# Kernel tuning notes

Measured on AMD Instinct MI355X. Metric: run time of the kernel, lower is better.

Reference implementation:

```python
import jax, jax.numpy as jnp
import numpy as np

B, D, NT, H, K = 4096, 112, 200, 512, 10
HID = 512
IN = 3 * D + NT + 1   # GRU input size = 537
M0 = H + 3 * D + NT   # MLP first-layer input = 1048


def setup_inputs() -> dict:
    key = jax.random.key(0)
    ks = jax.random.split(key, 9)
    def w(k, shape, fan):
        return jax.random.normal(k, shape, jnp.float32) / np.sqrt(fan).astype(np.float32)
    return {
        "z": jax.random.normal(ks[0], (B, D), jnp.float32),
        "c": jax.random.normal(ks[1], (B, D + NT), jnp.float32),
        "b": jax.random.uniform(ks[2], (B, D), jnp.float32),
        "m": jax.random.uniform(ks[3], (B, D), jnp.float32),
        "Wih": w(ks[4], (IN, 3 * H), IN),
        "Whh": w(ks[5], (H, 3 * H), H),
        "bih": jnp.zeros((3 * H,), jnp.float32),
        "bhh": jnp.zeros((3 * H,), jnp.float32),
        "W0": w(ks[6], (M0, HID), M0),
        "b0": jnp.zeros((HID,), jnp.float32),
        "W1": w(ks[7], (HID, HID), HID),
        "b1": jnp.zeros((HID,), jnp.float32),
        "W2": w(ks[8], (HID, 3 * K), HID),
        "b2": jnp.zeros((3 * K,), jnp.float32),
    }


def reference(z, c, b, m, Wih, Whh, bih, bhh, W0, b0, W1, b1, W2, b2):
    """AutoReg.logp: autoregressive GRU + MLP mixture-density head, gaussian base."""
    Bn = z.shape[0]
    const = jnp.concatenate([c, b, m], axis=1)          # [B, 3D+NT] fixed per step
    gi_const = const @ Wih[1:] + bih                    # input-proj of constant part
    w_z = Wih[0]                                        # [3H] weight for scalar z_t
    mlp_const = const @ W0[H:] + b0                     # const part of first MLP layer
    W0h = W0[:H]
    # teacher-forced previous-z sequence: z_0 = -1, then z[:, t-1]
    z_prev = jnp.concatenate([-jnp.ones((Bn, 1), z.dtype), z[:, :-1]], axis=1).T  # [D, B]

    def step(h, zt):  # h: [B,H], zt: [B]
        gi = zt[:, None] * w_z + gi_const               # [B, 3H]
        gh = h @ Whh + bhh
        ir, iz, inn = jnp.split(gi, 3, axis=1)
        hr, hz, hn = jnp.split(gh, 3, axis=1)
        r = jax.nn.sigmoid(ir + hr)
        u = jax.nn.sigmoid(iz + hz)
        n = jnp.tanh(inn + r * hn)
        h2 = (1.0 - u) * n + u * h                      # torch GRU update
        a = jnp.tanh(h2 @ W0h + mlp_const)              # Linear + Tanh on [h||c||b||m]
        a = jnp.tanh(a @ W1 + b1)
        p = a @ W2 + b2                                 # [B, 3K] mixture params
        return h2, p

    h0 = jnp.zeros((Bn, H), z.dtype)
    _, ps = jax.lax.scan(step, h0, z_prev)              # ps: [D, B, 3K]
    params = jnp.transpose(ps, (1, 0, 2))               # [B, D, 3K]

    logits, means, lsig = jnp.split(params, 3, axis=-1)
    sig = jnp.exp(lsig)
    t = z[..., None]
    log_norm = -lsig - 0.5 * np.float32(np.log(2.0 * np.pi))
    log_kern = -0.5 * jnp.square((t - means) / sig)
    ll = jax.nn.logsumexp(log_kern + log_norm + logits, axis=-1) \
         - jax.nn.logsumexp(logits, axis=-1)            # [B, D]

    query = m * (1.0 - b)
    mask = -jnp.sort(-query, axis=1)                    # descending sort values
    return jnp.sum(ll * mask, axis=1)                   # [B]
```

## Files before the change

kernel.cpp:

```cpp
#include <hip/hip_runtime.h>
#include <hip/hip_bf16.h>
#include <float.h>
#include <math.h>

#define BN   4096
#define DD   112
#define HH   512
#define G3   1536
#define CW   536
#define HIDD 512

typedef __attribute__((ext_vector_type(8))) short short8;
typedef __attribute__((ext_vector_type(4))) float float4v;

__device__ __forceinline__ unsigned short f2bf(float x) {
    __hip_bfloat16 h = __float2bfloat16(x);
    return *(unsigned short*)&h;
}

__global__ void build_const(const float* __restrict__ c, const float* __restrict__ b,
                            const float* __restrict__ m, float* __restrict__ out) {
    int idx = blockIdx.x * blockDim.x + threadIdx.x;
    if (idx >= BN * CW) return;
    int row = idx / CW, col = idx - row * CW;
    float v;
    if (col < 312)      v = c[row * 312 + col];
    else if (col < 424) v = b[row * 112 + (col - 312)];
    else                v = m[row * 112 + (col - 424)];
    out[idx] = v;
}

__global__ __launch_bounds__(256) void gemm_bias(const float* __restrict__ A,
        const float* __restrict__ W, const float* __restrict__ bias,
        float* __restrict__ C, int N) {
    __shared__ float As[8][64];
    __shared__ float Ws[8][64];
    const int tid = threadIdx.x;
    const int tx = tid & 15, ty = tid >> 4;
    const int rowBase = blockIdx.x * 64, colBase = blockIdx.y * 64;
    float acc[4][4] = {};
    for (int kb = 0; kb < CW; kb += 8) {
        int l = tid * 2;
        {
            int i = l >> 3, j = l & 7;
            As[j][i] = A[(rowBase + i) * CW + kb + j];
            int i2 = (l + 1) >> 3, j2 = (l + 1) & 7;
            As[j2][i2] = A[(rowBase + i2) * CW + kb + j2];
        }
        {
            int j = l >> 6, n = l & 63;
            Ws[j][n] = W[(kb + j) * N + colBase + n];
            int j2 = (l + 1) >> 6, n2 = (l + 1) & 63;
            Ws[j2][n2] = W[(kb + j2) * N + colBase + n2];
        }
        __syncthreads();
#pragma unroll
        for (int k = 0; k < 8; ++k) {
            float av[4], wv[4];
#pragma unroll
            for (int i = 0; i < 4; ++i) av[i] = As[k][ty * 4 + i];
#pragma unroll
            for (int j = 0; j < 4; ++j) wv[j] = Ws[k][tx * 4 + j];
#pragma unroll
            for (int i = 0; i < 4; ++i)
#pragma unroll
                for (int j = 0; j < 4; ++j) acc[i][j] += av[i] * wv[j];
        }
        __syncthreads();
    }
#pragma unroll
    for (int i = 0; i < 4; ++i) {
        int r = rowBase + ty * 4 + i;
#pragma unroll
        for (int j = 0; j < 4; ++j) {
            int cc = colBase + tx * 4 + j;
            C[r * N + cc] = acc[i][j] + bias[cc];
        }
    }
}

__global__ __launch_bounds__(256) void gemm_gicP(const float* __restrict__ A,
        const float* __restrict__ W, const float* __restrict__ bih,
        const float* __restrict__ bhh, float* __restrict__ gicP) {
    const int N = G3;
    __shared__ float As[8][64];
    __shared__ float Ws[8][64];
    const int tid = threadIdx.x;
    const int tx = tid & 15, ty = tid >> 4;
    const int rowBase = blockIdx.x * 64, colBase = blockIdx.y * 64;
    float acc[4][4] = {};
    for (int kb = 0; kb < CW; kb += 8) {
        int l = tid * 2;
        {
            int i = l >> 3, j = l & 7;
            As[j][i] = A[(rowBase + i) * CW + kb + j];
            int i2 = (l + 1) >> 3, j2 = (l + 1) & 7;
            As[j2][i2] = A[(rowBase + i2) * CW + kb + j2];
        }
        {
            int j = l >> 6, n = l & 63;
            Ws[j][n] = W[(kb + j) * N + colBase + n];
            int j2 = (l + 1) >> 6, n2 = (l + 1) & 63;
            Ws[j2][n2] = W[(kb + j2) * N + colBase + n2];
        }
        __syncthreads();
#pragma unroll
        for (int k = 0; k < 8; ++k) {
            float av[4], wv[4];
#pragma unroll
            for (int i = 0; i < 4; ++i) av[i] = As[k][ty * 4 + i];
#pragma unroll
            for (int j = 0; j < 4; ++j) wv[j] = Ws[k][tx * 4 + j];
#pragma unroll
            for (int i = 0; i < 4; ++i)
#pragma unroll
                for (int j = 0; j < 4; ++j) acc[i][j] += av[i] * wv[j];
        }
        __syncthreads();
    }
#pragma unroll
    for (int i = 0; i < 4; ++i) {
        int r = rowBase + ty * 4 + i;
        int ablock = r >> 5, mrem = r & 31, mt = mrem >> 4, mm = mrem & 15;
        int quad = mm >> 2, rg = mm & 3;
#pragma unroll
        for (int j = 0; j < 4; ++j) {
            int cc = colBase + tx * 4 + j;
            int g = cc >> 9, nrem = cc & 511, tile = nrem >> 4, l16 = nrem & 15;
            int wv = tile & 15, ii = tile >> 4;
            size_t off = ((((size_t)(ablock * 16 + wv) * 2 + ii) * 2 + mt) * 3 + g) * 256
                         + (quad * 16 + l16) * 4 + rg;
            gicP[off] = acc[i][j] + bih[cc] + ((g < 2) ? bhh[cc] : 0.0f);
        }
    }
}

__global__ void sort_mask(const float* __restrict__ b, const float* __restrict__ m,
                          float* __restrict__ maskbuf) {
    __shared__ float s[128];
    const int row = blockIdx.x, t = threadIdx.x;
    float v = -FLT_MAX;
    if (t < DD) v = m[row * DD + t] * (1.0f - b[row * DD + t]);
    s[t] = v;
    __syncthreads();
    for (int k = 2; k <= 128; k <<= 1) {
        for (int j = k >> 1; j > 0; j >>= 1) {
            int ixj = t ^ j;
            if (ixj > t) {
                bool up = ((t & k) == 0);
                float a = s[t], bb = s[ixj];
                if ((a > bb) == up) { s[t] = bb; s[ixj] = a; }
            }
            __syncthreads();
        }
    }
    if (t < DD) maskbuf[row * DD + t] = s[127 - t];
}

__global__ void pack_w(const float* __restrict__ src, unsigned short* __restrict__ dst,
                       int kchunks, int ldn, int ncols) {
    int bid = blockIdx.x;
    int nt = bid / kchunks, kc = bid - nt * kchunks;
    int lane = threadIdx.x;
    int quad = lane >> 4, l16 = lane & 15;
    int n = nt * 16 + l16;
    unsigned short v[8];
#pragma unroll
    for (int j = 0; j < 8; ++j) {
        int k = kc * 32 + quad * 8 + j;
        float f = (n < ncols) ? src[(size_t)k * ldn + n] : 0.0f;
        v[j] = f2bf(f);
    }
    unsigned short* p = dst + ((size_t)bid * 64 + lane) * 8;
#pragma unroll
    for (int j = 0; j < 8; ++j) p[j] = v[j];
}

__global__ __launch_bounds__(1024, 4) void gru_rec(
    const float* __restrict__ z, const float* __restrict__ Wih,
    const float* __restrict__ bhh, const float* __restrict__ gicP,
    const unsigned short* __restrict__ WhhP, unsigned short* __restrict__ h2g)
{
    __shared__ unsigned short h_bf[32 * 520];
    __shared__ float zbuf[113 * 32];

    const int tid = threadIdx.x;
    const int wave = tid >> 6, lane = tid & 63;
    const int quad = lane >> 4, l16 = lane & 15;
    const int rowBase = blockIdx.x * 32;

    for (int idx = tid; idx < 32 * 520; idx += 1024) h_bf[idx] = 0;
    for (int idx = tid; idx < 113 * 32; idx += 1024) {
        int tt = idx >> 5, r = idx & 31;
        zbuf[idx] = (tt == 0) ? -1.0f : z[(size_t)(rowBase + r) * DD + tt - 1];
    }

    int hcol[2];
    float wz0[2], wz1[2], wz2[2], bh2r[2];
#pragma unroll
    for (int i = 0; i < 2; ++i) {
        int hc = (wave + 16 * i) * 16 + l16;
        hcol[i] = hc;
        wz0[i] = Wih[hc]; wz1[i] = Wih[512 + hc]; wz2[i] = Wih[1024 + hc];
        bh2r[i] = bhh[1024 + hc];
    }
    float h_own[2][2][4];
#pragma unroll
    for (int i = 0; i < 2; ++i)
#pragma unroll
        for (int mt = 0; mt < 2; ++mt)
#pragma unroll
            for (int rg = 0; rg < 4; ++rg) h_own[i][mt][rg] = 0.0f;

    const float* gicW = gicP + (size_t)(blockIdx.x * 16 + wave) * 12 * 256;
    const short8* WhhF = (const short8*)WhhP;
    __syncthreads();

    for (int t = 0; t < DD; ++t) {
        float4v acc[3][2][2];
#pragma unroll
        for (int i = 0; i < 2; ++i)
#pragma unroll
            for (int mt = 0; mt < 2; ++mt) {
                acc[0][i][mt] = *(const float4v*)(gicW + ((i * 2 + mt) * 3 + 0) * 256 + lane * 4);
                acc[1][i][mt] = *(const float4v*)(gicW + ((i * 2 + mt) * 3 + 1) * 256 + lane * 4);
                acc[2][i][mt] = (float4v){0.f, 0.f, 0.f, 0.f};
            }
#pragma unroll 4
        for (int kc = 0; kc < 16; ++kc) {
            short8 af[2];
#pragma unroll
            for (int mt = 0; mt < 2; ++mt)
                af[mt] = *(const short8*)&h_bf[(mt * 16 + l16) * 520 + kc * 32 + quad * 8];
#pragma unroll
            for (int i = 0; i < 2; ++i) {
                int tile = wave + 16 * i;
#pragma unroll
                for (int g = 0; g < 3; ++g) {
                    short8 bf = WhhF[((tile + 32 * g) * 16 + kc) * 64 + lane];
#pragma unroll
                    for (int mt = 0; mt < 2; ++mt)
                        acc[g][i][mt] = __builtin_amdgcn_mfma_f32_16x16x32_bf16(af[mt], bf, acc[g][i][mt], 0, 0, 0);
                }
            }
        }
        __syncthreads();
#pragma unroll
        for (int i = 0; i < 2; ++i)
#pragma unroll
            for (int mt = 0; mt < 2; ++mt) {
                float4v gn = *(const float4v*)(gicW + ((i * 2 + mt) * 3 + 2) * 256 + lane * 4);
#pragma unroll
                for (int rg = 0; rg < 4; ++rg) {
                    int m = mt * 16 + quad * 4 + rg;
                    float zt = zbuf[t * 32 + m];
                    float r = 1.0f / (1.0f + __expf(-(acc[0][i][mt][rg] + zt * wz0[i])));
                    float u = 1.0f / (1.0f + __expf(-(acc[1][i][mt][rg] + zt * wz1[i])));
                    float xn = gn[rg] + zt * wz2[i] + r * (acc[2][i][mt][rg] + bh2r[i]);
                    float n = 1.0f - 2.0f / (__expf(2.0f * xn) + 1.0f);
                    float h2 = (1.0f - u) * n + u * h_own[i][mt][rg];
                    h_own[i][mt][rg] = h2;
                    h_bf[m * 520 + hcol[i]] = f2bf(h2);
                }
            }
        __syncthreads();
        {
            int flat = tid * 16;
            int r = flat >> 9, col = flat & 511;
            const uint4* src = (const uint4*)&h_bf[r * 520 + col];
            uint4 v0 = src[0], v1 = src[1];
            uint4* dst = (uint4*)&h2g[((size_t)(rowBase + r) * DD + t) * 512 + col];
            dst[0] = v0; dst[1] = v1;
        }
    }
}

__global__ __launch_bounds__(1024, 4) void head_mdn(
    const float* __restrict__ z, const float* __restrict__ b1,
    const float* __restrict__ b2, const float* __restrict__ mlp_const,
    const float* __restrict__ maskbuf, const unsigned short* __restrict__ h2g,
    const unsigned short* __restrict__ W0hP, const unsigned short* __restrict__ W1P,
    const unsigned short* __restrict__ W2P, float* __restrict__ out)
{
    __shared__ unsigned short h_bf[32 * 520];
    __shared__ unsigned short a_bf[32 * 520];
    __shared__ float pp[16 * 512];

    const int tid = threadIdx.x;
    const int wave = tid >> 6, lane = tid & 63;
    const int quad = lane >> 4, l16 = lane & 15;
    const int pr = tid >> 5, pc = tid & 31;
    const int bi = blockIdx.x / 7, ti = blockIdx.x - bi * 7;
    const int b0 = bi * 2, t0 = ti * 16;

    {
        int flat = tid * 16;
        int r = flat >> 9, col = flat & 511;
        int bb = b0 + (r >> 4), tt = t0 + (r & 15);
        const uint4* src = (const uint4*)&h2g[((size_t)bb * DD + tt) * 512 + col];
        uint4 v0 = src[0], v1 = src[1];
        uint4* dst = (uint4*)&h_bf[r * 520 + col];
        dst[0] = v0; dst[1] = v1;
    }
    int hcol[2];
    float b1c[2], mlc[2][2];
#pragma unroll
    for (int i = 0; i < 2; ++i) {
        int hc = (wave + 16 * i) * 16 + l16;
        hcol[i] = hc;
        b1c[i] = b1[hc];
#pragma unroll
        for (int mt = 0; mt < 2; ++mt) mlc[i][mt] = mlp_const[(size_t)(b0 + mt) * HIDD + hc];
    }
    const float b2v = (pc < 30) ? b2[pc] : 0.0f;
    const int mdn_mt = pr >> 4, mdn_m = pr & 15;
    const int ppofs = (mdn_mt * 8) * 512 + (pc >> 4) * 256
                      + ((mdn_m >> 2) * 16 + (pc & 15)) * 4 + (mdn_m & 3);

    const short8* W0hF = (const short8*)W0hP;
    const short8* W1F  = (const short8*)W1P;
    const short8* W2F  = (const short8*)W2P;
    __syncthreads();

    float4v acc1[2][2];
#pragma unroll
    for (int i = 0; i < 2; ++i)
#pragma unroll
        for (int mt = 0; mt < 2; ++mt)
            acc1[i][mt] = (float4v){mlc[i][mt], mlc[i][mt], mlc[i][mt], mlc[i][mt]};
#pragma unroll 4
    for (int kc = 0; kc < 16; ++kc) {
        short8 af0 = *(const short8*)&h_bf[l16 * 520 + kc * 32 + quad * 8];
        short8 af1 = *(const short8*)&h_bf[(16 + l16) * 520 + kc * 32 + quad * 8];
#pragma unroll
        for (int i = 0; i < 2; ++i) {
            short8 bf = W0hF[((wave + 16 * i) * 16 + kc) * 64 + lane];
            acc1[i][0] = __builtin_amdgcn_mfma_f32_16x16x32_bf16(af0, bf, acc1[i][0], 0, 0, 0);
            acc1[i][1] = __builtin_amdgcn_mfma_f32_16x16x32_bf16(af1, bf, acc1[i][1], 0, 0, 0);
        }
    }
#pragma unroll
    for (int i = 0; i < 2; ++i)
#pragma unroll
        for (int mt = 0; mt < 2; ++mt)
#pragma unroll
            for (int rg = 0; rg < 4; ++rg) {
                int m = mt * 16 + quad * 4 + rg;
                float x = acc1[i][mt][rg];
                a_bf[m * 520 + hcol[i]] = f2bf(1.0f - 2.0f / (__expf(2.0f * x) + 1.0f));
            }
    __syncthreads();
    float4v acc2[2][2];
#pragma unroll
    for (int i = 0; i < 2; ++i)
#pragma unroll
        for (int mt = 0; mt < 2; ++mt)
            acc2[i][mt] = (float4v){b1c[i], b1c[i], b1c[i], b1c[i]};
#pragma unroll 4
    for (int kc = 0; kc < 16; ++kc) {
        short8 af0 = *(const short8*)&a_bf[l16 * 520 + kc * 32 + quad * 8];
        short8 af1 = *(const short8*)&a_bf[(16 + l16) * 520 + kc * 32 + quad * 8];
#pragma unroll
        for (int i = 0; i < 2; ++i) {
            short8 bf = W1F[((wave + 16 * i) * 16 + kc) * 64 + lane];
            acc2[i][0] = __builtin_amdgcn_mfma_f32_16x16x32_bf16(af0, bf, acc2[i][0], 0, 0, 0);
            acc2[i][1] = __builtin_amdgcn_mfma_f32_16x16x32_bf16(af1, bf, acc2[i][1], 0, 0, 0);
        }
    }
    __syncthreads();
#pragma unroll
    for (int i = 0; i < 2; ++i)
#pragma unroll
        for (int mt = 0; mt < 2; ++mt)
#pragma unroll
            for (int rg = 0; rg < 4; ++rg) {
                int m = mt * 16 + quad * 4 + rg;
                float x = acc2[i][mt][rg];
                a_bf[m * 520 + hcol[i]] = f2bf(1.0f - 2.0f / (__expf(2.0f * x) + 1.0f));
            }
    __syncthreads();
    {
        const int mtw = wave >> 3;
        float4v ap0 = (float4v){0.f, 0.f, 0.f, 0.f}, ap1 = (float4v){0.f, 0.f, 0.f, 0.f};
#pragma unroll
        for (int kk = 0; kk < 2; ++kk) {
            int kc = (wave & 7) * 2 + kk;
            short8 af = *(const short8*)&a_bf[(mtw * 16 + l16) * 520 + kc * 32 + quad * 8];
            ap0 = __builtin_amdgcn_mfma_f32_16x16x32_bf16(af, W2F[(0 * 16 + kc) * 64 + lane], ap0, 0, 0, 0);
            ap1 = __builtin_amdgcn_mfma_f32_16x16x32_bf16(af, W2F[(1 * 16 + kc) * 64 + lane], ap1, 0, 0, 0);
        }
#pragma unroll
        for (int rg = 0; rg < 4; ++rg) {
            pp[wave * 512 + 0 * 256 + lane * 4 + rg] = ap0[rg];
            pp[wave * 512 + 1 * 256 + lane * 4 + rg] = ap1[rg];
        }
    }
    __syncthreads();
    float llm;
    {
        float pv = b2v;
#pragma unroll
        for (int w = 0; w < 8; ++w) pv += pp[ppofs + w * 512];
        const int half = lane & 32;
        float meanv = __shfl(pv, half + ((pc + 10) & 31), 64);
        float lsigv = __shfl(pv, half + ((pc + 20) & 31), 64);
        float e1, e2;
        if (pc < 10) {
            float ztar = z[(size_t)(b0 + mdn_mt) * DD + t0 + mdn_m];
            float invs = __expf(-lsigv);
            float dd = (ztar - meanv) * invs;
            e1 = -0.5f * dd * dd - lsigv - 0.91893853320467274f + pv;
            e2 = pv;
        } else { e1 = -FLT_MAX; e2 = -FLT_MAX; }
        float m1 = e1, m2 = e2;
#pragma unroll
        for (int off = 16; off > 0; off >>= 1) {
            m1 = fmaxf(m1, __shfl_xor(m1, off, 64));
            m2 = fmaxf(m2, __shfl_xor(m2, off, 64));
        }
        float s1 = (pc < 10) ? __expf(e1 - m1) : 0.0f;
        float s2 = (pc < 10) ? __expf(e2 - m2) : 0.0f;
#pragma unroll
        for (int off = 16; off > 0; off >>= 1) {
            s1 += __shfl_xor(s1, off, 64);
            s2 += __shfl_xor(s2, off, 64);
        }
        float ll = (m1 + __logf(s1)) - (m2 + __logf(s2));
        llm = ll * maskbuf[(size_t)(b0 + mdn_mt) * DD + t0 + mdn_m];
    }
    __syncthreads();
    if (pc == 0) pp[pr] = llm;
    __syncthreads();
    if (tid < 2) {
        float s = 0.0f;
#pragma unroll
        for (int j = 0; j < 16; ++j) s += pp[tid * 16 + j];
        atomicAdd(&out[b0 + tid], s);
    }
}

__global__ __launch_bounds__(1024, 4) void gru_mfma_r5(
    const float* __restrict__ z, const float* __restrict__ Wih,
    const float* __restrict__ bhh, const float* __restrict__ b1,
    const float* __restrict__ b2,
    const float* __restrict__ gi_const, const float* __restrict__ mlp_const,
    const float* __restrict__ maskbuf,
    const unsigned short* __restrict__ WhhP, const unsigned short* __restrict__ W0hP,
    const unsigned short* __restrict__ W1P, const unsigned short* __restrict__ W2P,
    float* __restrict__ out)
{
    __shared__ unsigned short h_bf[16 * 520];
    __shared__ unsigned short a_bf[16 * 520];
    __shared__ float pp[16 * 512];
    __shared__ float zbuf[113 * 16];
    __shared__ float mbuf[16 * 112];

    const int tid = threadIdx.x;
    const int wave = tid >> 6, lane = tid & 63;
    const int quad = lane >> 4, l16 = lane & 15;
    const int pr = tid >> 5, pc = tid & 31;
    const int rowBase = blockIdx.x * 16;

    for (int idx = tid; idx < 16 * 520; idx += 1024) h_bf[idx] = 0;
    for (int idx = tid; idx < 113 * 16; idx += 1024) {
        int tt = idx >> 4, r = idx & 15;
        zbuf[idx] = (tt == 0) ? -1.0f : z[(rowBase + r) * DD + tt - 1];
    }
    for (int idx = tid; idx < 16 * 112; idx += 1024) {
        int r = idx / DD, tt = idx - r * DD;
        mbuf[idx] = maskbuf[(rowBase + r) * DD + tt];
    }
    int hcol[2];
    float wz0[2], wz1[2], wz2[2], bh2r[2], b1c[2];
    float gic0[2][4], gic1[2][4], gic2[2][4], mlc[2][4];
    float h_own[2][4];
#pragma unroll
    for (int i = 0; i < 2; ++i) {
        int tile = wave + 16 * i;
        int hc = tile * 16 + l16;
        hcol[i] = hc;
        wz0[i] = Wih[hc]; wz1[i] = Wih[512 + hc]; wz2[i] = Wih[1024 + hc];
        float bh0 = bhh[hc], bh1 = bhh[512 + hc];
        bh2r[i] = bhh[1024 + hc];
        b1c[i] = b1[hc];
#pragma unroll
        for (int rg = 0; rg < 4; ++rg) {
            int m = quad * 4 + rg;
            const float* g = gi_const + (size_t)(rowBase + m) * G3;
            gic0[i][rg] = g[hc] + bh0;
            gic1[i][rg] = g[512 + hc] + bh1;
            gic2[i][rg] = g[1024 + hc];
            mlc[i][rg] = mlp_const[(size_t)(rowBase + m) * HIDD + hc];
            h_own[i][rg] = 0.0f;
        }
    }
    const float b2v = (pc < 30) ? b2[pc] : 0.0f;
    const int ppbase = (pc >> 4) * 256 + ((pr >> 2) * 16 + (pc & 15)) * 4 + (pr & 3);
    const short8* WhhF = (const short8*)WhhP;
    const short8* W0hF = (const short8*)W0hP;
    const short8* W1F  = (const short8*)W1P;
    const short8* W2F  = (const short8*)W2P;
    float llacc = 0.0f;
    __syncthreads();
    for (int t = 0; t < DD; ++t) {
        float4v accR[2], accU[2], accN[2];
#pragma unroll
        for (int i = 0; i < 2; ++i) {
            accR[i] = (float4v){gic0[i][0], gic0[i][1], gic0[i][2], gic0[i][3]};
            accU[i] = (float4v){gic1[i][0], gic1[i][1], gic1[i][2], gic1[i][3]};
            accN[i] = (float4v){0.f, 0.f, 0.f, 0.f};
        }
#pragma unroll 4
        for (int kc = 0; kc < 16; ++kc) {
            short8 af = *(const short8*)&h_bf[l16 * 520 + kc * 32 + quad * 8];
#pragma unroll
            for (int i = 0; i < 2; ++i) {
                int tile = wave + 16 * i;
                accR[i] = __builtin_amdgcn_mfma_f32_16x16x32_bf16(af, WhhF[(tile * 16 + kc) * 64 + lane], accR[i], 0, 0, 0);
                accU[i] = __builtin_amdgcn_mfma_f32_16x16x32_bf16(af, WhhF[((tile + 32) * 16 + kc) * 64 + lane], accU[i], 0, 0, 0);
                accN[i] = __builtin_amdgcn_mfma_f32_16x16x32_bf16(af, WhhF[((tile + 64) * 16 + kc) * 64 + lane], accN[i], 0, 0, 0);
            }
        }
        __syncthreads();
#pragma unroll
        for (int i = 0; i < 2; ++i) {
#pragma unroll
            for (int rg = 0; rg < 4; ++rg) {
                int m = quad * 4 + rg;
                float zt = zbuf[t * 16 + m];
                float r = 1.0f / (1.0f + __expf(-(accR[i][rg] + zt * wz0[i])));
                float u = 1.0f / (1.0f + __expf(-(accU[i][rg] + zt * wz1[i])));
                float xn = gic2[i][rg] + zt * wz2[i] + r * (accN[i][rg] + bh2r[i]);
                float n = 1.0f - 2.0f / (__expf(2.0f * xn) + 1.0f);
                float h2 = (1.0f - u) * n + u * h_own[i][rg];
                h_own[i][rg] = h2;
                h_bf[m * 520 + hcol[i]] = f2bf(h2);
            }
        }
        __syncthreads();
        float4v acc1[2];
#pragma unroll
        for (int i = 0; i < 2; ++i) acc1[i] = (float4v){mlc[i][0], mlc[i][1], mlc[i][2], mlc[i][3]};
#pragma unroll 4
        for (int kc = 0; kc < 16; ++kc) {
            short8 af = *(const short8*)&h_bf[l16 * 520 + kc * 32 + quad * 8];
#pragma unroll
            for (int i = 0; i < 2; ++i)
                acc1[i] = __builtin_amdgcn_mfma_f32_16x16x32_bf16(af, W0hF[((wave + 16 * i) * 16 + kc) * 64 + lane], acc1[i], 0, 0, 0);
        }
#pragma unroll
        for (int i = 0; i < 2; ++i)
#pragma unroll
            for (int rg = 0; rg < 4; ++rg) {
                int m = quad * 4 + rg;
                float x = acc1[i][rg];
                a_bf[m * 520 + hcol[i]] = f2bf(1.0f - 2.0f / (__expf(2.0f * x) + 1.0f));
            }
        __syncthreads();
        float4v acc2[2];
#pragma unroll
        for (int i = 0; i < 2; ++i) acc2[i] = (float4v){b1c[i], b1c[i], b1c[i], b1c[i]};
#pragma unroll 4
        for (int kc = 0; kc < 16; ++kc) {
            short8 af = *(const short8*)&a_bf[l16 * 520 + kc * 32 + quad * 8];
#pragma unroll
            for (int i = 0; i < 2; ++i)
                acc2[i] = __builtin_amdgcn_mfma_f32_16x16x32_bf16(af, W1F[((wave + 16 * i) * 16 + kc) * 64 + lane], acc2[i], 0, 0, 0);
        }
        __syncthreads();
#pragma unroll
        for (int i = 0; i < 2; ++i)
#pragma unroll
            for (int rg = 0; rg < 4; ++rg) {
                int m = quad * 4 + rg;
                float x = acc2[i][rg];
                a_bf[m * 520 + hcol[i]] = f2bf(1.0f - 2.0f / (__expf(2.0f * x) + 1.0f));
            }
        __syncthreads();
        {
            int kc = wave;
            short8 af = *(const short8*)&a_bf[l16 * 520 + kc * 32 + quad * 8];
            float4v ap0 = (float4v){0.f, 0.f, 0.f, 0.f}, ap1 = (float4v){0.f, 0.f, 0.f, 0.f};
            ap0 = __builtin_amdgcn_mfma_f32_16x16x32_bf16(af, W2F[(0 * 16 + kc) * 64 + lane], ap0, 0, 0, 0);
            ap1 = __builtin_amdgcn_mfma_f32_16x16x32_bf16(af, W2F[(1 * 16 + kc) * 64 + lane], ap1, 0, 0, 0);
#pragma unroll
            for (int rg = 0; rg < 4; ++rg) {
                pp[wave * 512 + 0 * 256 + lane * 4 + rg] = ap0[rg];
                pp[wave * 512 + 1 * 256 + lane * 4 + rg] = ap1[rg];
            }
        }
        __syncthreads();
        if (wave < 8) {
            float pv = b2v;
#pragma unroll
            for (int w = 0; w < 16; ++w) pv += pp[w * 512 + ppbase];
            const int half = lane & 32;
            float meanv = __shfl(pv, half + ((pc + 10) & 31), 64);
            float lsigv = __shfl(pv, half + ((pc + 20) & 31), 64);
            float e1, e2;
            if (pc < 10) {
                float ztar = zbuf[(t + 1) * 16 + pr];
                float invs = __expf(-lsigv);
                float dd = (ztar - meanv) * invs;
                e1 = -0.5f * dd * dd - lsigv - 0.91893853320467274f + pv;
                e2 = pv;
            } else { e1 = -FLT_MAX; e2 = -FLT_MAX; }
            float m1 = e1, m2 = e2;
#pragma unroll
            for (int off = 16; off > 0; off >>= 1) {
                m1 = fmaxf(m1, __shfl_xor(m1, off, 64));
                m2 = fmaxf(m2, __shfl_xor(m2, off, 64));
            }
            float s1 = (pc < 10) ? __expf(e1 - m1) : 0.0f;
            float s2 = (pc < 10) ? __expf(e2 - m2) : 0.0f;
#pragma unroll
            for (int off = 16; off > 0; off >>= 1) {
                s1 += __shfl_xor(s1, off, 64);
                s2 += __shfl_xor(s2, off, 64);
            }
            float ll = (m1 + __logf(s1)) - (m2 + __logf(s2));
            llacc += ll * mbuf[pr * 112 + t];
        }
    }
    if (wave < 8 && pc == 0) out[rowBase + pr] = llacc;
}

extern "C" void kernel_launch(void* const* d_in, const int* in_sizes, int n_in,
                              void* d_out, int out_size, void* d_ws, size_t ws_size,
                              hipStream_t stream) {
    const float* z   = (const float*)d_in[0];
    const float* c   = (const float*)d_in[1];
    const float* b   = (const float*)d_in[2];
    const float* m   = (const float*)d_in[3];
    const float* Wih = (const float*)d_in[4];
    const float* Whh = (const float*)d_in[5];
    const float* bih = (const float*)d_in[6];
    const float* bhh = (const float*)d_in[7];
    const float* W0  = (const float*)d_in[8];
    const float* b0  = (const float*)d_in[9];
    const float* W1  = (const float*)d_in[10];
    const float* b1  = (const float*)d_in[11];
    const float* W2  = (const float*)d_in[12];
    const float* b2  = (const float*)d_in[13];
    float* out = (float*)d_out;

    float* ws        = (float*)d_ws;
    float* constbuf  = ws;
    float* gi_region = constbuf + (size_t)BN * CW;
    float* mlp_const = gi_region + (size_t)BN * G3;
    float* maskbuf   = mlp_const + (size_t)BN * HIDD;
    unsigned short* WhhP = (unsigned short*)(maskbuf + (size_t)BN * DD);
    unsigned short* W0hP = WhhP + (size_t)96 * 16 * 512;
    unsigned short* W1P  = W0hP + (size_t)32 * 16 * 512;
    unsigned short* W2P  = W1P  + (size_t)32 * 16 * 512;
    unsigned short* h2g  = W2P + (size_t)2 * 16 * 512;

    const size_t need = (size_t)(constbuf ? 0 : 0)
        + ((size_t)BN * (CW + G3 + HIDD + DD)) * 4
        + ((size_t)(96 + 32 + 32 + 2) * 16 * 512) * 2
        + (size_t)BN * DD * 512 * 2;

    build_const<<<(BN * CW + 255) / 256, 256, 0, stream>>>(c, b, m, constbuf);
    dim3 g2(BN / 64, HIDD / 64);
    gemm_bias<<<g2, 256, 0, stream>>>(constbuf, W0 + (size_t)HH * HIDD, b0, mlp_const, HIDD);
    sort_mask<<<BN, 128, 0, stream>>>(b, m, maskbuf);
    pack_w<<<96 * 16, 64, 0, stream>>>(Whh, WhhP, 16, G3, G3);
    pack_w<<<32 * 16, 64, 0, stream>>>(W0,  W0hP, 16, HIDD, HIDD);
    pack_w<<<32 * 16, 64, 0, stream>>>(W1,  W1P,  16, HIDD, HIDD);
    pack_w<<<2 * 16, 64, 0, stream>>>(W2,  W2P,  16, 30, 30);

    dim3 g1(BN / 64, G3 / 64);
    if (ws_size >= need) {
        gemm_gicP<<<g1, 256, 0, stream>>>(constbuf, Wih + G3, bih, bhh, gi_region);
        hipMemsetAsync(d_out, 0, (size_t)out_size * sizeof(float), stream);
        gru_rec<<<BN / 32, 1024, 0, stream>>>(z, Wih, bhh, gi_region, WhhP, h2g);
        head_mdn<<<(BN / 2) * (DD / 16), 1024, 0, stream>>>(z, b1, b2, mlp_const,
                                                            maskbuf, h2g, W0hP, W1P, W2P, out);
    } else {
        gemm_bias<<<g1, 256, 0, stream>>>(constbuf, Wih + G3, bih, gi_region, G3);
        gru_mfma_r5<<<BN / 16, 1024, 0, stream>>>(z, Wih, bhh, b1, b2, gi_region,
                                                  mlp_const, maskbuf, WhhP, W0hP, W1P, W2P, out);
    }
}
```

Measured before the change: 3.152 ms.

## Chunk GRU recurrence over time with persistent hidden state and time-major h2 buffer

Replaces the single full-sequence GRU recurrence kernel with a chunked version that runs the time steps in slabs sized to the available workspace. Hidden state is saved to and restored from a global fp32 buffer between chunks, and the MLP/MDN head runs after each chunk. The recurrence blocks drop from 32 to 16 rows, with the gate constants held in registers instead of a pre-permuted gicP buffer, and h2 is stored time-major. The intent is to use the fast split recurrence+head path even when the workspace cannot hold all 112 steps, and to double the number of recurrence blocks. The cost is extra launches, hidden-state round trips, and half the MFMA reuse of Whh per block.

```diff
diff --git a/kernel.cpp b/kernel.cpp
--- a/kernel.cpp
+++ b/kernel.cpp
@@ -28,6 +28,11 @@
     else if (col < 424) v = b[row * 112 + (col - 312)];
     else                v = m[row * 112 + (col - 424)];
     out[idx] = v;
+}
+
+__global__ void zero_f32(float* __restrict__ p, int n) {
+    int i = blockIdx.x * blockDim.x + threadIdx.x;
+    if (i < n) p[i] = 0.0f;
 }
 
 __global__ __launch_bounds__(256) void gemm_bias(const float* __restrict__ A,
@@ -79,62 +84,6 @@
     }
 }
 
-__global__ __launch_bounds__(256) void gemm_gicP(const float* __restrict__ A,
-        const float* __restrict__ W, const float* __restrict__ bih,
-        const float* __restrict__ bhh, float* __restrict__ gicP) {
-    const int N = G3;
-    __shared__ float As[8][64];
-    __shared__ float Ws[8][64];
-    const int tid = threadIdx.x;
-    const int tx = tid & 15, ty = tid >> 4;
-    const int rowBase = blockIdx.x * 64, colBase = blockIdx.y * 64;
-    float acc[4][4] = {};
-    for (int kb = 0; kb < CW; kb += 8) {
-        int l = tid * 2;
-        {
-            int i = l >> 3, j = l & 7;
-            As[j][i] = A[(rowBase + i) * CW + kb + j];
-            int i2 = (l + 1) >> 3, j2 = (l + 1) & 7;
-            As[j2][i2] = A[(rowBase + i2) * CW + kb + j2];
-        }
-        {
-            int j = l >> 6, n = l & 63;
-            Ws[j][n] = W[(kb + j) * N + colBase + n];
-            int j2 = (l + 1) >> 6, n2 = (l + 1) & 63;
-            Ws[j2][n2] = W[(kb + j2) * N + colBase + n2];
-        }
-        __syncthreads();
-#pragma unroll
-        for (int k = 0; k < 8; ++k) {
-            float av[4], wv[4];
-#pragma unroll
-            for (int i = 0; i < 4; ++i) av[i] = As[k][ty * 4 + i];
-#pragma unroll
-            for (int j = 0; j < 4; ++j) wv[j] = Ws[k][tx * 4 + j];
-#pragma unroll
-            for (int i = 0; i < 4; ++i)
-#pragma unroll
-                for (int j = 0; j < 4; ++j) acc[i][j] += av[i] * wv[j];
-        }
-        __syncthreads();
-    }
-#pragma unroll
-    for (int i = 0; i < 4; ++i) {
-        int r = rowBase + ty * 4 + i;
-        int ablock = r >> 5, mrem = r & 31, mt = mrem >> 4, mm = mrem & 15;
-        int quad = mm >> 2, rg = mm & 3;
-#pragma unroll
-        for (int j = 0; j < 4; ++j) {
-            int cc = colBase + tx * 4 + j;
-            int g = cc >> 9, nrem = cc & 511, tile = nrem >> 4, l16 = nrem & 15;
-            int wv = tile & 15, ii = tile >> 4;
-            size_t off = ((((size_t)(ablock * 16 + wv) * 2 + ii) * 2 + mt) * 3 + g) * 256
-                         + (quad * 16 + l16) * 4 + rg;
-            gicP[off] = acc[i][j] + bih[cc] + ((g < 2) ? bhh[cc] : 0.0f);
-        }
-    }
-}
-
 __global__ void sort_mask(const float* __restrict__ b, const float* __restrict__ m,
                           float* __restrict__ maskbuf) {
     __shared__ float s[128];
@@ -176,103 +125,101 @@
     for (int j = 0; j < 8; ++j) p[j] = v[j];
 }
 
-__global__ __launch_bounds__(1024, 4) void gru_rec(
+__global__ __launch_bounds__(1024, 4) void gru_rec_chunk(
     const float* __restrict__ z, const float* __restrict__ Wih,
-    const float* __restrict__ bhh, const float* __restrict__ gicP,
-    const unsigned short* __restrict__ WhhP, unsigned short* __restrict__ h2g)
+    const float* __restrict__ bhh, const float* __restrict__ gi_const,
+    const unsigned short* __restrict__ WhhP,
+    float* __restrict__ hstate, unsigned short* __restrict__ h2g,
+    int t0, int tlen)
 {
-    __shared__ unsigned short h_bf[32 * 520];
-    __shared__ float zbuf[113 * 32];
+    __shared__ unsigned short h_bf[16 * 520];
+    __shared__ float zbuf[113 * 16];
 
     const int tid = threadIdx.x;
     const int wave = tid >> 6, lane = tid & 63;
     const int quad = lane >> 4, l16 = lane & 15;
-    const int rowBase = blockIdx.x * 32;
-
-    for (int idx = tid; idx < 32 * 520; idx += 1024) h_bf[idx] = 0;
-    for (int idx = tid; idx < 113 * 32; idx += 1024) {
-        int tt = idx >> 5, r = idx & 31;
-        zbuf[idx] = (tt == 0) ? -1.0f : z[(size_t)(rowBase + r) * DD + tt - 1];
+    const int rowBase = blockIdx.x * 16;
+
+    for (int idx = tid; idx < 113 * 16; idx += 1024) {
+        int tt = idx >> 4, r = idx & 15;
+        zbuf[idx] = (tt == 0) ? -1.0f : z[(rowBase + r) * DD + tt - 1];
     }
 
     int hcol[2];
     float wz0[2], wz1[2], wz2[2], bh2r[2];
+    float gic0[2][4], gic1[2][4], gic2[2][4];
+    float h_own[2][4];
 #pragma unroll
     for (int i = 0; i < 2; ++i) {
-        int hc = (wave + 16 * i) * 16 + l16;
+        int tile = wave + 16 * i;
+        int hc = tile * 16 + l16;
         hcol[i] = hc;
         wz0[i] = Wih[hc]; wz1[i] = Wih[512 + hc]; wz2[i] = Wih[1024 + hc];
+        float bh0 = bhh[hc], bh1 = bhh[512 + hc];
         bh2r[i] = bhh[1024 + hc];
-    }
-    float h_own[2][2][4];
-#pragma unroll
-    for (int i = 0; i < 2; ++i)
-#pragma unroll
-        for (int mt = 0; mt < 2; ++mt)
-#pragma unroll
-            for (int rg = 0; rg < 4; ++rg) h_own[i][mt][rg] = 0.0f;
-
-    const float* gicW = gicP + (size_t)(blockIdx.x * 16 + wave) * 12 * 256;
+#pragma unroll
+        for (int rg = 0; rg < 4; ++rg) {
+            int m = quad * 4 + rg;
+            const float* g = gi_const + (size_t)(rowBase + m) * G3;
+            gic0[i][rg] = g[hc] + bh0;
+            gic1[i][rg] = g[512 + hc] + bh1;
+            gic2[i][rg] = g[1024 + hc];
+            float hv = hstate[(size_t)(rowBase + m) * HH + hc];
+            h_own[i][rg] = hv;
+            h_bf[m * 520 + hc] = f2bf(hv);
+        }
+    }
     const short8* WhhF = (const short8*)WhhP;
     __syncthreads();
 
-    for (int t = 0; t < DD; ++t) {
-        float4v acc[3][2][2];
-#pragma unroll
-        for (int i = 0; i < 2; ++i)
-#pragma unroll
-            for (int mt = 0; mt < 2; ++mt) {
-                acc[0][i][mt] = *(const float4v*)(gicW + ((i * 2 + mt) * 3 + 0) * 256 + lane * 4);
-                acc[1][i][mt] = *(const float4v*)(gicW + ((i * 2 + mt) * 3 + 1) * 256 + lane * 4);
-                acc[2][i][mt] = (float4v){0.f, 0.f, 0.f, 0.f};
-            }
+    for (int tt = 0; tt < tlen; ++tt) {
+        const int t = t0 + tt;
+        float4v accR[2], accU[2], accN[2];
+#pragma unroll
+        for (int i = 0; i < 2; ++i) {
+            accR[i] = (float4v){gic0[i][0], gic0[i][1], gic0[i][2], gic0[i][3]};
+            accU[i] = (float4v){gic1[i][0], gic1[i][1], gic1[i][2], gic1[i][3]};
+            accN[i] = (float4v){0.f, 0.f, 0.f, 0.f};
+        }
 #pragma unroll 4
         for (int kc = 0; kc < 16; ++kc) {
-            short8 af[2];
-#pragma unroll
-            for (int mt = 0; mt < 2; ++mt)
-                af[mt] = *(const short8*)&h_bf[(mt * 16 + l16) * 520 + kc * 32 + quad * 8];
+            short8 af = *(const short8*)&h_bf[l16 * 520 + kc * 32 + quad * 8];
 #pragma unroll
             for (int i = 0; i < 2; ++i) {
                 int tile = wave + 16 * i;
-#pragma unroll
-                for (int g = 0; g < 3; ++g) {
-                    short8 bf = WhhF[((tile + 32 * g) * 16 + kc) * 64 + lane];
-#pragma unroll
-                    for (int mt = 0; mt < 2; ++mt)
-                        acc[g][i][mt] = __builtin_amdgcn_mfma_f32_16x16x32_bf16(af[mt], bf, acc[g][i][mt], 0, 0, 0);
-                }
-            }
-        }
-        __syncthreads();
-#pragma unroll
-        for (int i = 0; i < 2; ++i)
-#pragma unroll
-            for (int mt = 0; mt < 2; ++mt) {
-                float4v gn = *(const float4v*)(gicW + ((i * 2 + mt) * 3 + 2) * 256 + lane * 4);
-#pragma unroll
-                for (int rg = 0; rg < 4; ++rg) {
-                    int m = mt * 16 + quad * 4 + rg;
-                    float zt = zbuf[t * 32 + m];
-                    float r = 1.0f / (1.0f + __expf(-(acc[0][i][mt][rg] + zt * wz0[i])));
-                    float u = 1.0f / (1.0f + __expf(-(acc[1][i][mt][rg] + zt * wz1[i])));
-                    float xn = gn[rg] + zt * wz2[i] + r * (acc[2][i][mt][rg] + bh2r[i]);
-                    float n = 1.0f - 2.0f / (__expf(2.0f * xn) + 1.0f);
-                    float h2 = (1.0f - u) * n + u * h_own[i][mt][rg];
-                    h_own[i][mt][rg] = h2;
-                    h_bf[m * 520 + hcol[i]] = f2bf(h2);
-                }
-            }
+                accR[i] = __builtin_amdgcn_mfma_f32_16x16x32_bf16(af, WhhF[(tile * 16 + kc) * 64 + lane], accR[i], 0, 0, 0);
+                accU[i] = __builtin_amdgcn_mfma_f32_16x16x32_bf16(af, WhhF[((tile + 32) * 16 + kc) * 64 + lane], accU[i], 0, 0, 0);
+                accN[i] = __builtin_amdgcn_mfma_f32_16x16x32_bf16(af, WhhF[((tile + 64) * 16 + kc) * 64 + lane], accN[i], 0, 0, 0);
+            }
+        }
+        __syncthreads();
+#pragma unroll
+        for (int i = 0; i < 2; ++i) {
+#pragma unroll
+            for (int rg = 0; rg < 4; ++rg) {
+                int m = quad * 4 + rg;
+                float zt = zbuf[t * 16 + m];
+                float r = 1.0f / (1.0f + __expf(-(accR[i][rg] + zt * wz0[i])));
+                float u = 1.0f / (1.0f + __expf(-(accU[i][rg] + zt * wz1[i])));
+                float xn = gic2[i][rg] + zt * wz2[i] + r * (accN[i][rg] + bh2r[i]);
+                float n = 1.0f - 2.0f / (__expf(2.0f * xn) + 1.0f);
+                float h2 = (1.0f - u) * n + u * h_own[i][rg];
+                h_own[i][rg] = h2;
+                h_bf[m * 520 + hcol[i]] = f2bf(h2);
+            }
+        }
         __syncthreads();
         {
-            int flat = tid * 16;
-            int r = flat >> 9, col = flat & 511;
-            const uint4* src = (const uint4*)&h_bf[r * 520 + col];
-            uint4 v0 = src[0], v1 = src[1];
-            uint4* dst = (uint4*)&h2g[((size_t)(rowBase + r) * DD + t) * 512 + col];
-            dst[0] = v0; dst[1] = v1;
-        }
-    }
+            int col = (lane) * 8;
+            uint4 v = *(const uint4*)&h_bf[wave * 520 + col];
+            *(uint4*)&h2g[((size_t)tt * BN + rowBase + wave) * 512 + col] = v;
+        }
+    }
+#pragma unroll
+    for (int i = 0; i < 2; ++i)
+#pragma unroll
+        for (int rg = 0; rg < 4; ++rg)
+            hstate[(size_t)(rowBase + quad * 4 + rg) * HH + hcol[i]] = h_own[i][rg];
 }
 
 __global__ __launch_bounds__(1024, 4) void head_mdn(
@@ -280,7 +227,7 @@
     const float* __restrict__ b2, const float* __restrict__ mlp_const,
     const float* __restrict__ maskbuf, const unsigned short* __restrict__ h2g,
     const unsigned short* __restrict__ W0hP, const unsigned short* __restrict__ W1P,
-    const unsigned short* __restrict__ W2P, float* __restrict__ out)
+    const unsigned short* __restrict__ W2P, float* __restrict__ out, int t0)
 {
     __shared__ unsigned short h_bf[32 * 520];
     __shared__ unsigned short a_bf[32 * 520];
@@ -290,15 +237,15 @@
     const int wave = tid >> 6, lane = tid & 63;
     const int quad = lane >> 4, l16 = lane & 15;
     const int pr = tid >> 5, pc = tid & 31;
-    const int bi = blockIdx.x / 7, ti = blockIdx.x - bi * 7;
-    const int b0 = bi * 2, t0 = ti * 16;
+    const int b0 = blockIdx.x * 2;
+    const int tg = blockIdx.y;
 
     {
         int flat = tid * 16;
         int r = flat >> 9, col = flat & 511;
-        int bb = b0 + (r >> 4), tt = t0 + (r & 15);
-        const uint4* src = (const uint4*)&h2g[((size_t)bb * DD + tt) * 512 + col];
-        uint4 v0 = src[0], v1 = src[1];
+        int bb = b0 + (r >> 4), trel = tg * 16 + (r & 15);
+        uint4 v0 = ((const uint4*)&h2g[((size_t)trel * BN + bb) * 512 + col])[0];
+        uint4 v1 = ((const uint4*)&h2g[((size_t)trel * BN + bb) * 512 + col])[1];
         uint4* dst = (uint4*)&h_bf[r * 520 + col];
         dst[0] = v0; dst[1] = v1;
     }
@@ -406,7 +353,7 @@
         float lsigv = __shfl(pv, half + ((pc + 20) & 31), 64);
         float e1, e2;
         if (pc < 10) {
-            float ztar = z[(size_t)(b0 + mdn_mt) * DD + t0 + mdn_m];
+            float ztar = z[(size_t)(b0 + mdn_mt) * DD + t0 + tg * 16 + mdn_m];
             float invs = __expf(-lsigv);
             float dd = (ztar - meanv) * invs;
             e1 = -0.5f * dd * dd - lsigv - 0.91893853320467274f + pv;
@@ -426,7 +373,7 @@
             s2 += __shfl_xor(s2, off, 64);
         }
         float ll = (m1 + __logf(s1)) - (m2 + __logf(s2));
-        llm = ll * maskbuf[(size_t)(b0 + mdn_mt) * DD + t0 + mdn_m];
+        llm = ll * maskbuf[(size_t)(b0 + mdn_mt) * DD + t0 + tg * 16 + mdn_m];
     }
     __syncthreads();
     if (pc == 0) pp[pr] = llm;
@@ -646,21 +593,30 @@
 
     float* ws        = (float*)d_ws;
     float* constbuf  = ws;
-    float* gi_region = constbuf + (size_t)BN * CW;
-    float* mlp_const = gi_region + (size_t)BN * G3;
+    float* gi_const  = constbuf + (size_t)BN * CW;
+    float* mlp_const = gi_const + (size_t)BN * G3;
     float* maskbuf   = mlp_const + (size_t)BN * HIDD;
     unsigned short* WhhP = (unsigned short*)(maskbuf + (size_t)BN * DD);
     unsigned short* W0hP = WhhP + (size_t)96 * 16 * 512;
     unsigned short* W1P  = W0hP + (size_t)32 * 16 * 512;
     unsigned short* W2P  = W1P  + (size_t)32 * 16 * 512;
-    unsigned short* h2g  = W2P + (size_t)2 * 16 * 512;
-
-    const size_t need = (size_t)(constbuf ? 0 : 0)
-        + ((size_t)BN * (CW + G3 + HIDD + DD)) * 4
-        + ((size_t)(96 + 32 + 32 + 2) * 16 * 512) * 2
-        + (size_t)BN * DD * 512 * 2;
+    float* hstate        = (float*)(W2P + (size_t)2 * 16 * 512);
+    unsigned short* h2g  = (unsigned short*)(hstate + (size_t)BN * HH);
+
+    const size_t base = (size_t)BN * (CW + G3 + HIDD + DD) * 4
+                      + (size_t)(96 + 32 + 32 + 2) * 16 * 512 * 2
+                      + (size_t)BN * HH * 4;
+    const size_t slab_per_t = (size_t)BN * 512 * 2;
+    int TC = 0;
+    if (ws_size > base) {
+        TC = (int)((ws_size - base) / slab_per_t);
+        TC = (TC / 16) * 16;
+        if (TC > DD) TC = DD;
+    }
 
     build_const<<<(BN * CW + 255) / 256, 256, 0, stream>>>(c, b, m, constbuf);
+    dim3 g1(BN / 64, G3 / 64);
+    gemm_bias<<<g1, 256, 0, stream>>>(constbuf, Wih + G3, bih, gi_const, G3);
     dim3 g2(BN / 64, HIDD / 64);
     gemm_bias<<<g2, 256, 0, stream>>>(constbuf, W0 + (size_t)HH * HIDD, b0, mlp_const, HIDD);
     sort_mask<<<BN, 128, 0, stream>>>(b, m, maskbuf);
@@ -669,16 +625,19 @@
     pack_w<<<32 * 16, 64, 0, stream>>>(W1,  W1P,  16, HIDD, HIDD);
     pack_w<<<2 * 16, 64, 0, stream>>>(W2,  W2P,  16, 30, 30);
 
-    dim3 g1(BN / 64, G3 / 64);
-    if (ws_size >= need) {
-        gemm_gicP<<<g1, 256, 0, stream>>>(constbuf, Wih + G3, bih, bhh, gi_region);
-        hipMemsetAsync(d_out, 0, (size_t)out_size * sizeof(float), stream);
-        gru_rec<<<BN / 32, 1024, 0, stream>>>(z, Wih, bhh, gi_region, WhhP, h2g);
-        head_mdn<<<(BN / 2) * (DD / 16), 1024, 0, stream>>>(z, b1, b2, mlp_const,
-                                                            maskbuf, h2g, W0hP, W1P, W2P, out);
+    if (TC >= 16) {
+        zero_f32<<<(BN * HH + 255) / 256, 256, 0, stream>>>(hstate, BN * HH);
+        zero_f32<<<(BN + 255) / 256, 256, 0, stream>>>(out, BN);
+        for (int t0 = 0; t0 < DD; t0 += TC) {
+            int tlen = DD - t0 < TC ? DD - t0 : TC;
+            gru_rec_chunk<<<BN / 16, 1024, 0, stream>>>(z, Wih, bhh, gi_const, WhhP,
+                                                        hstate, h2g, t0, tlen);
+            dim3 gh(BN / 2, tlen / 16);
+            head_mdn<<<gh, 1024, 0, stream>>>(z, b1, b2, mlp_const, maskbuf, h2g,
+                                              W0hP, W1P, W2P, out, t0);
+        }
     } else {
-        gemm_bias<<<g1, 256, 0, stream>>>(constbuf, Wih + G3, bih, gi_region, G3);
-        gru_mfma_r5<<<BN / 16, 1024, 0, stream>>>(z, Wih, bhh, b1, b2, gi_region,
+        gru_mfma_r5<<<BN / 16, 1024, 0, stream>>>(z, Wih, bhh, b1, b2, gi_const,
                                                   mlp_const, maskbuf, WhhP, W0hP, W1P, W2P, out);
     }
 }
```

After: 2.971 ms. -5.7%, faster.
